# Optimization experiments

Hardware: AMD Instinct MI355X
Metric: run time of the kernel (lower is better)

Reference implementation:

```python
import jax, jax.numpy as jnp
import numpy as np

B, T, H, A = 64, 512, 1024, 300


def setup_inputs() -> dict:
    key = jax.random.key(0)
    ks = jax.random.split(key, 12)
    s = 0.02  # weight init scale
    return {
        "hidden": jax.random.normal(ks[0], (B, T, H), jnp.float32),
        "aspect": jax.random.normal(ks[1], (B, 1, A), jnp.float32),
        # torch Linear stores weight as [out_features, in_features]
        "W_h": jax.random.normal(ks[2], (H, H), jnp.float32) * s,
        "b_h": jax.random.normal(ks[3], (H,), jnp.float32) * s,
        "W_v": jax.random.normal(ks[4], (A, A), jnp.float32) * s,
        "b_v": jax.random.normal(ks[5], (A,), jnp.float32) * s,
        "w_w": jax.random.normal(ks[6], (1, H + A), jnp.float32) * s,
        "w_b": jax.random.normal(ks[7], (1,), jnp.float32) * s,
        "W_p": jax.random.normal(ks[8], (H, H), jnp.float32) * s,
        "b_p": jax.random.normal(ks[9], (H,), jnp.float32) * s,
        "W_x": jax.random.normal(ks[10], (H, H), jnp.float32) * s,
        "b_x": jax.random.normal(ks[11], (H,), jnp.float32) * s,
    }


def reference(hidden, aspect, W_h, b_h, W_v, b_v, w_w, w_b, W_p, b_p, W_x, b_x):
    # transformed aspect: [B, 1, A], repeated along seq dim -> [B, T, A]
    tv = aspect @ W_v.T + b_v
    rep_v = jnp.broadcast_to(tv, (hidden.shape[0], hidden.shape[1], tv.shape[-1]))
    # M = tanh(concat(W_h(hidden), repeated_v)) : [B, T, H+A]
    M = jnp.tanh(jnp.concatenate([hidden @ W_h.T + b_h, rep_v], axis=-1))
    # additive attention scores -> softmax over T
    scores = jnp.einsum("bts,os->bto", M, w_w)[..., 0] + w_b[0]  # [B, T]
    alpha = jax.nn.softmax(scores, axis=-1)
    # weighted sum r = alpha^T @ hidden : [B, 1, H]
    r = jnp.einsum("bt,bth->bh", alpha, hidden)[:, None, :]
    # NOTE: faithful to original torch broadcasting quirk:
    # [B,1,H] + [B,H] broadcasts to [B,B,H]
    output = jnp.tanh((r @ W_p.T + b_p) + (hidden[:, -1, :] @ W_x.T + b_x))
    return output
```

## Files before the change

kernel.cpp:

```cpp
#include <hip/hip_runtime.h>
#include <hip/hip_bf16.h>
#include <stdint.h>

#define B_DIM 64
#define T_DIM 512
#define H_DIM 1024
#define K_DIM 1024
#define M_DIM (B_DIM * T_DIM)
#define GM_BK 64
#define IG 4

typedef __bf16 bf16x8 __attribute__((ext_vector_type(8)));
typedef float f32x4 __attribute__((ext_vector_type(4)));

__device__ __forceinline__ float tanh_fast(float x) {
  float e = __expf(2.0f * x);
  return 1.0f - 2.0f / (e + 1.0f);
}

__device__ __forceinline__ float bf2f(unsigned short u) {
  return __uint_as_float(((unsigned int)u) << 16);
}

__device__ __forceinline__ void async_cp16(const void* gp, void* lp) {
  __builtin_amdgcn_global_load_lds(
      reinterpret_cast<const __attribute__((address_space(1))) uint32_t*>(
          reinterpret_cast<uintptr_t>(gp)),
      reinterpret_cast<__attribute__((address_space(3))) uint32_t*>(
          reinterpret_cast<uintptr_t>(lp)),
      16, 0, 0);
}

__device__ __forceinline__ void cvt4(const float4& v, uint2* dst) {
  union { __bf16 b[4]; uint2 u; } o;
  o.b[0] = (__bf16)v.x; o.b[1] = (__bf16)v.y; o.b[2] = (__bf16)v.z; o.b[3] = (__bf16)v.w;
  *dst = o.u;
}

#define STRIDE_NTHR (2048 * 256)
__global__ void prep_kernel(const float* __restrict__ hidden, __bf16* __restrict__ hidBf,
                            const float* __restrict__ Wh, __bf16* __restrict__ whBf) {
  const int gt = blockIdx.x * 256 + threadIdx.x;
  const float4* hs = reinterpret_cast<const float4*>(hidden);
  uint2* hd = reinterpret_cast<uint2*>(hidBf);
#pragma unroll 4
  for (int i = gt; i < 8388608; i += STRIDE_NTHR) {
    cvt4(hs[i], &hd[i]);
  }
  const float4* wsrc = reinterpret_cast<const float4*>(Wh);
  uint2* wd = reinterpret_cast<uint2*>(whBf);
  if (gt < 262144) cvt4(wsrc[gt], &wd[gt]);
}

__global__ __launch_bounds__(256, 2) void gemm_scores_kernel(
    const __bf16* __restrict__ A, const __bf16* __restrict__ Bm,
    const float* __restrict__ bh, const float* __restrict__ ww,
    float* __restrict__ scoresP, int m_base) {
  __shared__ __attribute__((aligned(16))) __bf16 lA[256 * GM_BK];
  __shared__ __attribute__((aligned(16))) __bf16 lB[128 * GM_BK];
  const int tid = threadIdx.x;
  const int bid = blockIdx.x;
  const int m0 = (bid & 63) * 256 + m_base;
  const int nIdx = bid >> 6;
  const int n0 = nIdx * 128;
  const int wv = tid >> 6;
  const int lane = tid & 63;
  const int wm = wv & 1, wn = wv >> 1;
  const int r16 = lane & 15, quad = lane >> 4;
  f32x4 acc[8][4] = {};
  const __bf16* gA[8]; __bf16* lAd[8];
#pragma unroll
  for (int j = 0; j < 8; ++j) {
    int c = j * 256 + tid;
    int row = c >> 3;
    int p = c & 7;
    int kc = p ^ ((row >> 1) & 7);
    gA[j] = A + (size_t)(m0 + row) * K_DIM + kc * 8;
    lAd[j] = &lA[c * 8];
  }
  const __bf16* gB[4]; __bf16* lBd[4];
#pragma unroll
  for (int j = 0; j < 4; ++j) {
    int c = j * 256 + tid;
    int row = c >> 3;
    int p = c & 7;
    int kc = p ^ ((row >> 1) & 7);
    gB[j] = Bm + (size_t)(n0 + row) * K_DIM + kc * 8;
    lBd[j] = &lB[c * 8];
  }
  const int sw = r16 >> 1;
  const __bf16* pa[2]; const __bf16* pb[2];
#pragma unroll
  for (int kk = 0; kk < 2; ++kk) {
    pa[kk] = &lA[(wm * 128 + r16) * GM_BK + ((kk * 4 + quad) ^ sw) * 8];
    pb[kk] = &lB[(wn * 64 + r16) * GM_BK + ((kk * 4 + quad) ^ sw) * 8];
  }
#pragma unroll
  for (int k0 = 0; k0 < K_DIM; k0 += GM_BK) {
#pragma unroll
    for (int j = 0; j < 8; ++j) async_cp16(gA[j] + k0, lAd[j]);
#pragma unroll
    for (int j = 0; j < 4; ++j) async_cp16(gB[j] + k0, lBd[j]);
    __syncthreads();
#pragma unroll
    for (int kk = 0; kk < 2; ++kk) {
      bf16x8 bfr[4];
#pragma unroll
      for (int ni = 0; ni < 4; ++ni)
        bfr[ni] = *reinterpret_cast<const bf16x8*>(pb[kk] + ni * 16 * GM_BK);
      bf16x8 af[8];
#pragma unroll
      for (int mi = 0; mi < 8; ++mi)
        af[mi] = *reinterpret_cast<const bf16x8*>(pa[kk] + mi * 16 * GM_BK);
#pragma unroll
      for (int mi = 0; mi < 8; ++mi)
#pragma unroll
        for (int ni = 0; ni < 4; ++ni)
          acc[mi][ni] = __builtin_amdgcn_mfma_f32_16x16x32_bf16(af[mi], bfr[ni], acc[mi][ni], 0, 0, 0);
    }
    __syncthreads();
  }
  float* sBuf = reinterpret_cast<float*>(lA);
  float bhv[4], wwv[4];
#pragma unroll
  for (int ni = 0; ni < 4; ++ni) {
    int n = n0 + wn * 64 + ni * 16 + r16;
    bhv[ni] = bh[n];
    wwv[ni] = ww[n];
  }
#pragma unroll
  for (int mi = 0; mi < 8; ++mi) {
#pragma unroll
    for (int rg = 0; rg < 4; ++rg) {
      float s = 0.f;
#pragma unroll
      for (int ni = 0; ni < 4; ++ni)
        s += tanh_fast(acc[mi][ni][rg] + bhv[ni]) * wwv[ni];
      s += __shfl_xor(s, 1, 16);
      s += __shfl_xor(s, 2, 16);
      s += __shfl_xor(s, 4, 16);
      s += __shfl_xor(s, 8, 16);
      if (r16 == 0) {
        int lm = wm * 128 + mi * 16 + quad * 4 + rg;
        sBuf[wn * 256 + lm] = s;
      }
    }
  }
  __syncthreads();
  scoresP[nIdx * M_DIM + m0 + tid] = sBuf[tid] + sBuf[256 + tid];
}

__global__ void wsum_kernel(const float* __restrict__ scoresP,
                            const __bf16* __restrict__ hiddenBf,
                            float* __restrict__ r8) {
  __shared__ float sc[512];
  __shared__ float al[64];
  __shared__ float red[8];
  const int bid = blockIdx.x, tid = threadIdx.x;
  const int b = bid >> 3, tc = bid & 7;
  const int wv = tid >> 6, lane = tid & 63;
  float v0 = 0.f, v1 = 0.f;
#pragma unroll
  for (int p = 0; p < 8; ++p) {
    v0 += scoresP[p * M_DIM + b * T_DIM + tid];
    v1 += scoresP[p * M_DIM + b * T_DIM + 256 + tid];
  }
  sc[tid] = v0;
  sc[tid + 256] = v1;
  float mx = fmaxf(v0, v1);
#pragma unroll
  for (int off = 1; off < 64; off <<= 1) mx = fmaxf(mx, __shfl_xor(mx, off, 64));
  if (lane == 0) red[wv] = mx;
  __syncthreads();
  mx = fmaxf(fmaxf(red[0], red[1]), fmaxf(red[2], red[3]));
  float e0 = __expf(v0 - mx), e1 = __expf(v1 - mx);
  float s = e0 + e1;
#pragma unroll
  for (int off = 1; off < 64; off <<= 1) s += __shfl_xor(s, off, 64);
  if (lane == 0) red[4 + wv] = s;
  __syncthreads();
  float inv = 1.0f / (red[4] + red[5] + red[6] + red[7]);
  if (tid < 64) al[tid] = __expf(sc[tc * 64 + tid] - mx) * inv;
  __syncthreads();
  const __bf16* hp = hiddenBf + (size_t)b * T_DIM * H_DIM + (size_t)tc * 64 * H_DIM + tid * 4;
  float4 acc = make_float4(0.f, 0.f, 0.f, 0.f);
#pragma unroll 8
  for (int t = 0; t < 64; ++t) {
    float a = al[t];
    ushort4 u = *reinterpret_cast<const ushort4*>(hp + (size_t)t * H_DIM);
    acc.x += a * bf2f(u.x);
    acc.y += a * bf2f(u.y);
    acc.z += a * bf2f(u.z);
    acc.w += a * bf2f(u.w);
  }
  *reinterpret_cast<float4*>(r8 + (size_t)(b * 8 + tc) * H_DIM + tid * 4) = acc;
}

__global__ void rowvec2_kernel(const float* __restrict__ r8,
                               const float* __restrict__ hidden,
                               const float* __restrict__ W_p, const float* __restrict__ b_p,
                               const float* __restrict__ W_x, const float* __restrict__ b_x,
                               float* __restrict__ rp, float* __restrict__ xq) {
  __shared__ __attribute__((aligned(16))) float sv[IG][H_DIM];
  const int h0 = blockIdx.x * 64;
  const int i0 = blockIdx.y * IG;
  const int which = blockIdx.z;
  const int tid = threadIdx.x;
  const float* W = which ? W_x : W_p;
  const float* bias = which ? b_x : b_p;
  float* dst = which ? xq : rp;
  if (which == 0) {
#pragma unroll
    for (int ii = 0; ii < IG; ++ii) {
      const float* src = r8 + (size_t)(i0 + ii) * 8 * H_DIM + tid * 4;
      float4 a = *reinterpret_cast<const float4*>(src);
#pragma unroll
      for (int tc = 1; tc < 8; ++tc) {
        float4 v = *reinterpret_cast<const float4*>(src + (size_t)tc * H_DIM);
        a.x += v.x; a.y += v.y; a.z += v.z; a.w += v.w;
      }
      *reinterpret_cast<float4*>(&sv[ii][tid * 4]) = a;
    }
  } else {
#pragma unroll
    for (int ii = 0; ii < IG; ++ii) {
      const float* src = hidden + (size_t)(i0 + ii) * T_DIM * H_DIM +
                         (size_t)(T_DIM - 1) * H_DIM + tid * 4;
      *reinterpret_cast<float4*>(&sv[ii][tid * 4]) = *reinterpret_cast<const float4*>(src);
    }
  }
  __syncthreads();
  const int hl = tid >> 2;
  const int kq = tid & 3;
  const float* wr = W + (size_t)(h0 + hl) * H_DIM + kq * 4;
  float acc[IG] = {};
#pragma unroll 8
  for (int j = 0; j < 64; ++j) {
    float4 w4 = *reinterpret_cast<const float4*>(wr + j * 16);
#pragma unroll
    for (int ii = 0; ii < IG; ++ii) {
      float4 s4 = *reinterpret_cast<const float4*>(&sv[ii][kq * 4 + j * 16]);
      acc[ii] += w4.x * s4.x + w4.y * s4.y + w4.z * s4.z + w4.w * s4.w;
    }
  }
#pragma unroll
  for (int ii = 0; ii < IG; ++ii) {
    acc[ii] += __shfl_xor(acc[ii], 1, 4);
    acc[ii] += __shfl_xor(acc[ii], 2, 4);
  }
  if (kq == 0) {
    float bb = bias[h0 + hl];
#pragma unroll
    for (int ii = 0; ii < IG; ++ii)
      dst[(size_t)(i0 + ii) * H_DIM + h0 + hl] = acc[ii] + bb;
  }
}

__global__ void final_kernel(const float* __restrict__ rp, const float* __restrict__ xq,
                             float* __restrict__ out) {
  const int gt = blockIdx.x * 256 + threadIdx.x;
#pragma unroll
  for (int idx = gt; idx < 1048576; idx += STRIDE_NTHR) {
    int e = idx * 4;
    int i = e >> 16;
    int j = (e >> 10) & 63;
    int h = e & 1023;
    float4 a = *reinterpret_cast<const float4*>(&rp[i * H_DIM + h]);
    float4 b = *reinterpret_cast<const float4*>(&xq[j * H_DIM + h]);
    float4 o;
    o.x = tanh_fast(a.x + b.x);
    o.y = tanh_fast(a.y + b.y);
    o.z = tanh_fast(a.z + b.z);
    o.w = tanh_fast(a.w + b.w);
    *reinterpret_cast<float4*>(&out[e]) = o;
  }
}

extern "C" void kernel_launch(void* const* d_in, const int* in_sizes, int n_in,
                              void* d_out, int out_size, void* d_ws, size_t ws_size,
                              hipStream_t stream) {
  const float* hidden = (const float*)d_in[0];
  const float* W_h = (const float*)d_in[2];
  const float* b_h = (const float*)d_in[3];
  const float* w_w = (const float*)d_in[6];
  const float* W_p = (const float*)d_in[8];
  const float* b_p = (const float*)d_in[9];
  const float* W_x = (const float*)d_in[10];
  const float* b_x = (const float*)d_in[11];
  float* out = (float*)d_out;

  char* ws = (char*)d_ws;
  __bf16* hidBf = (__bf16*)ws;
  __bf16* whBf = (__bf16*)(ws + 67108864);
  float* r8 = (float*)(ws + 67108864);
  float* scoresP = (float*)(ws + 69206016);
  float* rpB = (float*)ws;
  float* xqB = (float*)(ws + 262144);

  prep_kernel<<<2048, 256, 0, stream>>>(hidden, hidBf, W_h, whBf);

  gemm_scores_kernel<<<512, 256, 0, stream>>>(hidBf, whBf, b_h, w_w, scoresP, 0);
  gemm_scores_kernel<<<512, 256, 0, stream>>>(hidBf, whBf, b_h, w_w, scoresP, 16384);

  wsum_kernel<<<512, 256, 0, stream>>>(scoresP, hidBf, r8);

  rowvec2_kernel<<<dim3(H_DIM / 64, B_DIM / IG, 2), 256, 0, stream>>>(
      r8, hidden, W_p, b_p, W_x, b_x, rpB, xqB);

  final_kernel<<<2048, 256, 0, stream>>>(rpB, xqB, out);
}
```

Measured before the change: 354.2 us.

## Rewrite scores GEMM as 256x256-tile kernel with 4-stage async LDS pipeline

Replaces the two single-buffered 256x128 GEMM launches with one 512-thread kernel that computes 256x256 output tiles. It streams K in 32-wide slices through a 4-deep ring of LDS buffers, with explicit vmcnt waits and one barrier per slice, and interleaves the global-to-LDS loads with MFMA groups under raised wave priority. The goal is to hide global load latency behind compute, halve the barrier count, and halve the partial-score planes that wsum has to reduce. In exchange it uses more LDS per block and depends on hand-counted vmcnt values being correct.

```diff
diff --git a/kernel.cpp b/kernel.cpp
--- a/kernel.cpp
+++ b/kernel.cpp
@@ -7,7 +7,6 @@
 #define H_DIM 1024
 #define K_DIM 1024
 #define M_DIM (B_DIM * T_DIM)
-#define GM_BK 64
 #define IG 4
 
 typedef __bf16 bf16x8 __attribute__((ext_vector_type(8)));
@@ -52,74 +51,110 @@
   if (gt < 262144) cvt4(wsrc[gt], &wd[gt]);
 }
 
-__global__ __launch_bounds__(256, 2) void gemm_scores_kernel(
+__global__ __launch_bounds__(512, 2) void gemm8_kernel(
     const __bf16* __restrict__ A, const __bf16* __restrict__ Bm,
     const float* __restrict__ bh, const float* __restrict__ ww,
-    float* __restrict__ scoresP, int m_base) {
-  __shared__ __attribute__((aligned(16))) __bf16 lA[256 * GM_BK];
-  __shared__ __attribute__((aligned(16))) __bf16 lB[128 * GM_BK];
+    float* __restrict__ scoresP) {
+  __shared__ __attribute__((aligned(16))) __bf16 lA[4 * 8192];
+  __shared__ __attribute__((aligned(16))) __bf16 lB[4 * 8192];
   const int tid = threadIdx.x;
   const int bid = blockIdx.x;
-  const int m0 = (bid & 63) * 256 + m_base;
-  const int nIdx = bid >> 6;
-  const int n0 = nIdx * 128;
-  const int wv = tid >> 6;
-  const int lane = tid & 63;
-  const int wm = wv & 1, wn = wv >> 1;
+  const int m0 = (bid & 127) * 256;
+  const int nIdx = bid >> 7;
+  const int n0 = nIdx * 256;
+  const int wid = tid >> 6, lane = tid & 63;
+  const int wm = wid >> 2, wn = wid & 3;
   const int r16 = lane & 15, quad = lane >> 4;
+  const int sw2 = (r16 >> 1) & 3;
+
+  int srow[2], skc[2];
+#pragma unroll
+  for (int j = 0; j < 2; ++j) {
+    int c = j * 512 + tid;
+    srow[j] = c >> 2;
+    skc[j] = (c & 3) ^ ((srow[j] >> 1) & 3);
+  }
+  int offA[8], offB[4];
+#pragma unroll
+  for (int mi = 0; mi < 8; ++mi)
+    offA[mi] = (wm * 128 + mi * 16 + r16) * 32 + (quad ^ sw2) * 8;
+#pragma unroll
+  for (int ni = 0; ni < 4; ++ni)
+    offB[ni] = (wn * 64 + ni * 16 + r16) * 32 + (quad ^ sw2) * 8;
+
+  auto stageA = [&](int ts, int bs) {
+#pragma unroll
+    for (int j = 0; j < 2; ++j)
+      async_cp16(A + (size_t)(m0 + srow[j]) * K_DIM + ts * 32 + skc[j] * 8,
+                 lA + bs * 8192 + (j * 512 + tid) * 8);
+  };
+  auto stageB = [&](int ts, int bs) {
+#pragma unroll
+    for (int j = 0; j < 2; ++j)
+      async_cp16(Bm + (size_t)(n0 + srow[j]) * K_DIM + ts * 32 + skc[j] * 8,
+                 lB + bs * 8192 + (j * 512 + tid) * 8);
+  };
+
   f32x4 acc[8][4] = {};
-  const __bf16* gA[8]; __bf16* lAd[8];
-#pragma unroll
-  for (int j = 0; j < 8; ++j) {
-    int c = j * 256 + tid;
-    int row = c >> 3;
-    int p = c & 7;
-    int kc = p ^ ((row >> 1) & 7);
-    gA[j] = A + (size_t)(m0 + row) * K_DIM + kc * 8;
-    lAd[j] = &lA[c * 8];
-  }
-  const __bf16* gB[4]; __bf16* lBd[4];
-#pragma unroll
-  for (int j = 0; j < 4; ++j) {
-    int c = j * 256 + tid;
-    int row = c >> 3;
-    int p = c & 7;
-    int kc = p ^ ((row >> 1) & 7);
-    gB[j] = Bm + (size_t)(n0 + row) * K_DIM + kc * 8;
-    lBd[j] = &lB[c * 8];
-  }
-  const int sw = r16 >> 1;
-  const __bf16* pa[2]; const __bf16* pb[2];
-#pragma unroll
-  for (int kk = 0; kk < 2; ++kk) {
-    pa[kk] = &lA[(wm * 128 + r16) * GM_BK + ((kk * 4 + quad) ^ sw) * 8];
-    pb[kk] = &lB[(wn * 64 + r16) * GM_BK + ((kk * 4 + quad) ^ sw) * 8];
-  }
-#pragma unroll
-  for (int k0 = 0; k0 < K_DIM; k0 += GM_BK) {
-#pragma unroll
-    for (int j = 0; j < 8; ++j) async_cp16(gA[j] + k0, lAd[j]);
-#pragma unroll
-    for (int j = 0; j < 4; ++j) async_cp16(gB[j] + k0, lBd[j]);
-    __syncthreads();
-#pragma unroll
-    for (int kk = 0; kk < 2; ++kk) {
-      bf16x8 bfr[4];
+
+  auto tile = [&](int t, bool st) {
+    const __bf16* lab = lA + (t & 3) * 8192;
+    const __bf16* lbb = lB + (t & 3) * 8192;
+    if (st) stageA(t + 3, (t + 3) & 3);
+    bf16x8 bf[4];
+#pragma unroll
+    for (int ni = 0; ni < 4; ++ni)
+      bf[ni] = *reinterpret_cast<const bf16x8*>(lbb + offB[ni]);
+    bf16x8 af0[4];
+#pragma unroll
+    for (int mi = 0; mi < 4; ++mi)
+      af0[mi] = *reinterpret_cast<const bf16x8*>(lab + offA[mi]);
+    __builtin_amdgcn_s_setprio(1);
+#pragma unroll
+    for (int mi = 0; mi < 4; ++mi)
 #pragma unroll
       for (int ni = 0; ni < 4; ++ni)
-        bfr[ni] = *reinterpret_cast<const bf16x8*>(pb[kk] + ni * 16 * GM_BK);
-      bf16x8 af[8];
-#pragma unroll
-      for (int mi = 0; mi < 8; ++mi)
-        af[mi] = *reinterpret_cast<const bf16x8*>(pa[kk] + mi * 16 * GM_BK);
-#pragma unroll
-      for (int mi = 0; mi < 8; ++mi)
-#pragma unroll
-        for (int ni = 0; ni < 4; ++ni)
-          acc[mi][ni] = __builtin_amdgcn_mfma_f32_16x16x32_bf16(af[mi], bfr[ni], acc[mi][ni], 0, 0, 0);
-    }
-    __syncthreads();
-  }
+        acc[mi][ni] = __builtin_amdgcn_mfma_f32_16x16x32_bf16(af0[mi], bf[ni], acc[mi][ni], 0, 0, 0);
+    __builtin_amdgcn_s_setprio(0);
+    if (st) stageB(t + 3, (t + 3) & 3);
+    bf16x8 af1[4];
+#pragma unroll
+    for (int mi = 0; mi < 4; ++mi)
+      af1[mi] = *reinterpret_cast<const bf16x8*>(lab + offA[4 + mi]);
+    __builtin_amdgcn_s_setprio(1);
+#pragma unroll
+    for (int mi = 0; mi < 4; ++mi)
+#pragma unroll
+      for (int ni = 0; ni < 4; ++ni)
+        acc[4 + mi][ni] = __builtin_amdgcn_mfma_f32_16x16x32_bf16(af1[mi], bf[ni], acc[4 + mi][ni], 0, 0, 0);
+    __builtin_amdgcn_s_setprio(0);
+  };
+
+  stageA(0, 0); stageB(0, 0);
+  stageA(1, 1); stageB(1, 1);
+  stageA(2, 2); stageB(2, 2);
+
+#pragma unroll 1
+  for (int t = 0; t < 29; ++t) {
+    asm volatile("s_waitcnt vmcnt(8)" ::: "memory");
+    __builtin_amdgcn_s_barrier();
+    __builtin_amdgcn_sched_barrier(0);
+    tile(t, true);
+  }
+  asm volatile("s_waitcnt vmcnt(8)" ::: "memory");
+  __builtin_amdgcn_s_barrier();
+  __builtin_amdgcn_sched_barrier(0);
+  tile(29, false);
+  asm volatile("s_waitcnt vmcnt(4)" ::: "memory");
+  __builtin_amdgcn_s_barrier();
+  __builtin_amdgcn_sched_barrier(0);
+  tile(30, false);
+  asm volatile("s_waitcnt vmcnt(0)" ::: "memory");
+  __builtin_amdgcn_s_barrier();
+  __builtin_amdgcn_sched_barrier(0);
+  tile(31, false);
+  __syncthreads();
+
   float* sBuf = reinterpret_cast<float*>(lA);
   float bhv[4], wwv[4];
 #pragma unroll
@@ -140,14 +175,14 @@
       s += __shfl_xor(s, 2, 16);
       s += __shfl_xor(s, 4, 16);
       s += __shfl_xor(s, 8, 16);
-      if (r16 == 0) {
-        int lm = wm * 128 + mi * 16 + quad * 4 + rg;
-        sBuf[wn * 256 + lm] = s;
-      }
+      if (r16 == 0) sBuf[wn * 256 + wm * 128 + mi * 16 + quad * 4 + rg] = s;
     }
   }
   __syncthreads();
-  scoresP[nIdx * M_DIM + m0 + tid] = sBuf[tid] + sBuf[256 + tid];
+  if (tid < 256) {
+    scoresP[nIdx * M_DIM + m0 + tid] =
+        sBuf[tid] + sBuf[256 + tid] + sBuf[512 + tid] + sBuf[768 + tid];
+  }
 }
 
 __global__ void wsum_kernel(const float* __restrict__ scoresP,
@@ -161,7 +196,7 @@
   const int wv = tid >> 6, lane = tid & 63;
   float v0 = 0.f, v1 = 0.f;
 #pragma unroll
-  for (int p = 0; p < 8; ++p) {
+  for (int p = 0; p < 4; ++p) {
     v0 += scoresP[p * M_DIM + b * T_DIM + tid];
     v1 += scoresP[p * M_DIM + b * T_DIM + 256 + tid];
   }
@@ -299,8 +334,7 @@
 
   prep_kernel<<<2048, 256, 0, stream>>>(hidden, hidBf, W_h, whBf);
 
-  gemm_scores_kernel<<<512, 256, 0, stream>>>(hidBf, whBf, b_h, w_w, scoresP, 0);
-  gemm_scores_kernel<<<512, 256, 0, stream>>>(hidBf, whBf, b_h, w_w, scoresP, 16384);
+  gemm8_kernel<<<512, 512, 0, stream>>>(hidBf, whBf, b_h, w_w, scoresP);
 
   wsum_kernel<<<512, 256, 0, stream>>>(scoresP, hidBf, r8);
 
```

Result: no change. 357.9 us (+1.0%).
